# Performance work log

Measured on AMD Instinct MI355X. Metric: run time of the kernel, lower is better.

Reference implementation:

```python
import jax, jax.numpy as jnp
import numpy as np
from jax import lax

EPS = 1e-5

def _dsconv(x, dw, pw, g, b, m, v, relu):
    # x: [B,C,H,W]; dw: [C,1,3,3] depthwise; pw: [C,C,1,1] pointwise; eval-mode BN
    C = x.shape[1]
    y = lax.conv_general_dilated(x, dw, (1, 1), 'SAME', feature_group_count=C)
    y = lax.conv_general_dilated(y, pw, (1, 1), 'SAME')
    scale = (g * lax.rsqrt(v + EPS))[None, :, None, None]
    y = y * scale + (b - m * g * lax.rsqrt(v + EPS))[None, :, None, None]
    return jnp.maximum(y, 0.0) if relu else y

def _attention(x, wq, bq, wk, bk, wv, bv, gamma):
    b, c, h, w = x.shape
    n = h * w
    xf = x.reshape(b, c, n)                      # [B,C,N]
    q = jnp.einsum('oc,bcn->bon', wq, xf) + bq[None, :, None]   # [B,C/8,N]
    k = jnp.einsum('oc,bcn->bon', wk, xf) + bk[None, :, None]   # [B,C/8,N]
    v = jnp.einsum('oc,bcn->bon', wv, xf) + bv[None, :, None]   # [B,C,N]
    logits = jnp.einsum('bdm,bdn->bmn', q, k)    # q^T k, [B,N,N]
    attn = jax.nn.softmax(logits, axis=2)
    out = jnp.einsum('bcn,bmn->bcm', v, attn).reshape(b, c, h, w)
    return gamma[0] * out + x

def setup_inputs() -> dict:
    key = jax.random.key(0)
    ks = jax.random.split(key, 20)
    B, C, H, W = 64, 256, 32, 32
    C8 = C // 8
    rn = lambda k, s, sc: (jax.random.normal(k, s, dtype=jnp.float32) * sc)
    return {
        'x': rn(ks[0], (B, C, H, W), 1.0),
        'dw1': rn(ks[1], (C, 1, 3, 3), 0.2),
        'pw1': rn(ks[2], (C, C, 1, 1), 0.06),
        'bn1_g': jax.random.uniform(ks[3], (C,), jnp.float32, 0.5, 1.5),
        'bn1_b': rn(ks[4], (C,), 0.1),
        'bn1_m': rn(ks[5], (C,), 0.1),
        'bn1_v': jax.random.uniform(ks[6], (C,), jnp.float32, 0.5, 1.5),
        'dw2': rn(ks[7], (C, 1, 3, 3), 0.2),
        'pw2': rn(ks[8], (C, C, 1, 1), 0.06),
        'bn2_g': jax.random.uniform(ks[9], (C,), jnp.float32, 0.5, 1.5),
        'bn2_b': rn(ks[10], (C,), 0.1),
        'bn2_m': rn(ks[11], (C,), 0.1),
        'bn2_v': jax.random.uniform(ks[12], (C,), jnp.float32, 0.5, 1.5),
        'wq': rn(ks[13], (C8, C), 0.06),
        'bq': rn(ks[14], (C8,), 0.02),
        'wk': rn(ks[15], (C8, C), 0.06),
        'bk': rn(ks[16], (C8,), 0.02),
        'wv': rn(ks[17], (C, C), 0.06),
        'bv': rn(ks[18], (C,), 0.02),
        'gamma': rn(ks[19], (1,), 0.5),
    }

def reference(x, dw1, pw1, bn1_g, bn1_b, bn1_m, bn1_v,
              dw2, pw2, bn2_g, bn2_b, bn2_m, bn2_v,
              wq, bq, wk, bk, wv, bv, gamma):
    out = _dsconv(x, dw1, pw1, bn1_g, bn1_b, bn1_m, bn1_v, relu=True)
    out = _dsconv(out, dw2, pw2, bn2_g, bn2_b, bn2_m, bn2_v, relu=False)
    out = _attention(out + x, wq, bq, wk, bk, wv, bv, gamma)
    return jnp.maximum(out, 0.0)
```

## Files before the change

### kernel.cpp

```cpp
#include <hip/hip_runtime.h>
#include <cstdint>
#include <cstddef>

#define B_ 64
#define C_ 256
#define N_ 1024
#define LOG2E 1.4426950408889634f

typedef short v8s __attribute__((ext_vector_type(8)));
typedef float v4f __attribute__((ext_vector_type(4)));
typedef unsigned int u32;
typedef unsigned short u16;

__device__ __forceinline__ float bf2f(u16 u) {
  return __uint_as_float(((u32)u) << 16);
}
__device__ __forceinline__ u16 f2bf(float f) {
  u32 x = __float_as_uint(f);
  x += 0x7fffu + ((x >> 16) & 1u);
  return (u16)(x >> 16);
}
__device__ __forceinline__ u32 pack2(float a, float b) {
  return (u32)f2bf(a) | ((u32)f2bf(b) << 16);
}

typedef __attribute__((address_space(3))) unsigned int lds_as_t;
typedef __attribute__((address_space(1))) const unsigned int glb_as_t;
__device__ __forceinline__ void ld_lds16(const u16* g, u16* l) {
  __builtin_amdgcn_global_load_lds((glb_as_t*)g, (lds_as_t*)l, 16, 0, 0);
}

__global__ __launch_bounds__(256) void prep(
    const float* __restrict__ g1, const float* __restrict__ b1,
    const float* __restrict__ m1, const float* __restrict__ v1,
    const float* __restrict__ g2, const float* __restrict__ b2,
    const float* __restrict__ m2, const float* __restrict__ v2,
    const float* __restrict__ wq, const float* __restrict__ bq,
    const float* __restrict__ wk, const float* __restrict__ bk,
    const float* __restrict__ wv, const float* __restrict__ bv,
    const float* __restrict__ pw1, const float* __restrict__ pw2,
    const float* __restrict__ dw1, const float* __restrict__ dw2,
    float* __restrict__ scale1, float* __restrict__ shift1,
    float* __restrict__ scale2, float* __restrict__ shift2,
    float* __restrict__ dwT1, float* __restrict__ dwT2,
    u16* __restrict__ pw1b, u16* __restrict__ pw2b, u16* __restrict__ wcatb,
    float* __restrict__ bcat) {
  const int gt = blockIdx.x * 256 + threadIdx.x;
  if (gt < 256) {
    float s1 = g1[gt] * rsqrtf(v1[gt] + 1e-5f);
    scale1[gt] = s1;
    shift1[gt] = b1[gt] - m1[gt] * s1;
    float s2 = g2[gt] * rsqrtf(v2[gt] + 1e-5f);
    scale2[gt] = s2;
    shift2[gt] = b2[gt] - m2[gt] * s2;
  }
  if (gt < 320)
    bcat[gt] = (gt < 32) ? bq[gt] * LOG2E
                         : (gt < 64) ? bk[gt - 32] : bv[gt - 64];
  if (gt < 2304) {
    dwT1[(gt % 9) * 256 + gt / 9] = dw1[gt];
    dwT2[(gt % 9) * 256 + gt / 9] = dw2[gt];
  }
  for (int e = gt; e < 65536; e += 16384) {
    pw1b[e] = f2bf(pw1[e]);
    pw2b[e] = f2bf(pw2[e]);
  }
  for (int e = gt; e < 81920; e += 16384) {
    const int o = e >> 8;
    float w = (o < 32) ? wq[e] * LOG2E
                       : (o < 64) ? wk[e - 8192] : wv[e - 16384];
    wcatb[e] = f2bf(w);
  }
}

__global__ __launch_bounds__(256) void transpose_x(const float* __restrict__ x,
                                                   u16* __restrict__ xt) {
  __shared__ float t[64][65];
  const int b = blockIdx.z, c0 = blockIdx.y * 64, n0 = blockIdx.x * 64;
  const float* xp = x + ((size_t)b * C_ + c0) * N_ + n0;
  const int tn = threadIdx.x & 63, tc = threadIdx.x >> 6;
#pragma unroll
  for (int i = 0; i < 16; ++i)
    t[tc + 4 * i][tn] = xp[(size_t)(tc + 4 * i) * N_ + tn];
  __syncthreads();
  u16* op = xt + ((size_t)b * N_ + n0) * C_ + c0;
  const int oc = threadIdx.x & 63, on = threadIdx.x >> 6;
#pragma unroll
  for (int i = 0; i < 16; ++i)
    op[(size_t)(on + 4 * i) * C_ + oc] = f2bf(t[oc][on + 4 * i]);
}

__global__ __launch_bounds__(256) void dw_nhwc(const u16* __restrict__ src,
                                               const float* __restrict__ wT,
                                               u16* __restrict__ dst) {
  __shared__ float wl[9][256];
  const int b = blockIdx.y;
  for (int e = threadIdx.x; e < 2304; e += 256) wl[e >> 8][e & 255] = wT[e];
  __syncthreads();
  const int pl = threadIdx.x >> 5, c0 = (threadIdx.x & 31) * 8;
  const int p = blockIdx.x * 8 + pl;
  const int h = p >> 5, wx = p & 31;
  const u16* sp = src + (size_t)b * N_ * C_;
  float acc[8] = {0.f, 0.f, 0.f, 0.f, 0.f, 0.f, 0.f, 0.f};
#pragma unroll
  for (int dh = -1; dh <= 1; ++dh) {
    const int hh = h + dh;
    if (hh < 0 || hh > 31) continue;
#pragma unroll
    for (int dx = -1; dx <= 1; ++dx) {
      const int ww = wx + dx;
      if (ww < 0 || ww > 31) continue;
      const int k = (dh + 1) * 3 + (dx + 1);
      const uint4 v = *(const uint4*)(sp + (size_t)(hh * 32 + ww) * C_ + c0);
      const u32 vv[4] = {v.x, v.y, v.z, v.w};
#pragma unroll
      for (int j = 0; j < 4; ++j) {
        acc[2 * j] += bf2f((u16)(vv[j] & 0xffffu)) * wl[k][c0 + 2 * j];
        acc[2 * j + 1] += bf2f((u16)(vv[j] >> 16)) * wl[k][c0 + 2 * j + 1];
      }
    }
  }
  uint4 o4;
  o4.x = pack2(acc[0], acc[1]);
  o4.y = pack2(acc[2], acc[3]);
  o4.z = pack2(acc[4], acc[5]);
  o4.w = pack2(acc[6], acc[7]);
  *(uint4*)(dst + ((size_t)b * N_ + p) * C_ + c0) = o4;
}

template <int EPI>
__global__ __launch_bounds__(256) void gemm(
    const u16* __restrict__ X, const u16* __restrict__ W,
    const float* __restrict__ scale, const float* __restrict__ shift,
    const u16* __restrict__ resid, u16* __restrict__ Y, u16* __restrict__ Y2) {
  __shared__ u16 smem[17408];
  u16(*Xs)[64] = (u16(*)[64])smem;
  u16(*Ws)[64] = (u16(*)[64])(smem + 8192);
  u16(*Ys)[136] = (u16(*)[136])smem;

  const int tid = threadIdx.x;
  const int b = blockIdx.z;
  const int n0 = blockIdx.x * 128, o0 = blockIdx.y * 128;
  const int wid = tid >> 6, lane = tid & 63;
  const int wn = wid & 1, wo = wid >> 1;
  const int l15 = lane & 15, l4 = lane >> 4;
  const int lr = lane >> 3, lc = (lane & 7) * 8;

  v4f acc[4][4];
#pragma unroll
  for (int i = 0; i < 4; ++i)
#pragma unroll
    for (int j = 0; j < 4; ++j) acc[i][j] = v4f{0.f, 0.f, 0.f, 0.f};

  for (int k0 = 0; k0 < C_; k0 += 64) {
#pragma unroll
    for (int g = 0; g < 4; ++g) {
      const int base = wid * 32 + g * 8;
      ld_lds16(X + ((size_t)b * N_ + n0 + base + lr) * C_ + k0 + lc,
               &Xs[base][0]);
      int wr = o0 + base + lr;
      if (EPI == 2 && wr > 319) wr = 319;
      ld_lds16(W + (size_t)wr * C_ + k0 + lc, &Ws[base][0]);
    }
    __syncthreads();
#pragma unroll
    for (int ks = 0; ks < 2; ++ks) {
      v8s af[4], bf4[4];
#pragma unroll
      for (int f = 0; f < 4; ++f) {
        if constexpr (EPI != 2) {
          af[f] = *(const v8s*)&Ws[wo * 64 + f * 16 + l15][ks * 32 + l4 * 8];
          bf4[f] = *(const v8s*)&Xs[wn * 64 + f * 16 + l15][ks * 32 + l4 * 8];
        } else {
          af[f] = *(const v8s*)&Xs[wn * 64 + f * 16 + l15][ks * 32 + l4 * 8];
          bf4[f] = *(const v8s*)&Ws[wo * 64 + f * 16 + l15][ks * 32 + l4 * 8];
        }
      }
#pragma unroll
      for (int i = 0; i < 4; ++i)
#pragma unroll
        for (int j = 0; j < 4; ++j)
          acc[i][j] = __builtin_amdgcn_mfma_f32_16x16x32_bf16(
              af[i], bf4[j], acc[i][j], 0, 0, 0);
    }
    __syncthreads();
  }

  if constexpr (EPI != 2) {
#pragma unroll
    for (int i = 0; i < 4; ++i) {
      const int oL = wo * 64 + i * 16 + l4 * 4;
      const int o = o0 + oL;
      const float4 sc = *(const float4*)&scale[o];
      const float4 sh = *(const float4*)&shift[o];
#pragma unroll
      for (int j = 0; j < 4; ++j) {
        const int nL = wn * 64 + j * 16 + l15;
        float y0 = acc[i][j][0] * sc.x + sh.x;
        float y1 = acc[i][j][1] * sc.y + sh.y;
        float y2 = acc[i][j][2] * sc.z + sh.z;
        float y3 = acc[i][j][3] * sc.w + sh.w;
        if constexpr (EPI == 0) {
          y0 = fmaxf(y0, 0.f);
          y1 = fmaxf(y1, 0.f);
          y2 = fmaxf(y2, 0.f);
          y3 = fmaxf(y3, 0.f);
        } else {
          const uint2 rb =
              *(const uint2*)(resid + ((size_t)b * N_ + n0 + nL) * C_ + o);
          y0 += bf2f((u16)(rb.x & 0xffffu));
          y1 += bf2f((u16)(rb.x >> 16));
          y2 += bf2f((u16)(rb.y & 0xffffu));
          y3 += bf2f((u16)(rb.y >> 16));
        }
        uint2 st;
        st.x = pack2(y0, y1);
        st.y = pack2(y2, y3);
        *(uint2*)&Ys[nL][oL] = st;
      }
    }
    __syncthreads();
#pragma unroll
    for (int s = 0; s < 8; ++s) {
      const int nL = s * 16 + (tid >> 4);
      const int slot = tid & 15;
      const uint4 v = *(const uint4*)&Ys[nL][slot * 8];
      *(uint4*)&Y[((size_t)b * N_ + n0 + nL) * C_ + o0 + slot * 8] = v;
    }
  } else {
    float bj[4];
#pragma unroll
    for (int j = 0; j < 4; ++j) {
      int o = o0 + wo * 64 + j * 16 + l15;
      bj[j] = shift[o > 319 ? 319 : o];
    }
    if (o0 == 0 && wo == 0) {
#pragma unroll
      for (int i = 0; i < 4; ++i) {
        const int nB = n0 + wn * 64 + i * 16 + l4 * 4;
#pragma unroll
        for (int j = 0; j < 4; ++j) {
          const int o = j * 16 + l15;
#pragma unroll
          for (int r = 0; r < 4; ++r)
            Y[((size_t)b * N_ + nB + r) * 64 + o] = f2bf(acc[i][j][r] + bj[j]);
        }
      }
    } else {
#pragma unroll
      for (int i = 0; i < 4; ++i) {
        const int nL = wn * 64 + i * 16 + l4 * 4;
#pragma unroll
        for (int j = 0; j < 4; ++j) {
          const int oL = wo * 64 + j * 16 + l15;
          uint2 st;
          st.x = pack2(acc[i][j][0] + bj[j], acc[i][j][1] + bj[j]);
          st.y = pack2(acc[i][j][2] + bj[j], acc[i][j][3] + bj[j]);
          *(uint2*)&Ys[oL][nL] = st;
        }
      }
    }
    __syncthreads();
#pragma unroll
    for (int s = 0; s < 8; ++s) {
      const int oL = s * 16 + (tid >> 4);
      const int c = o0 + oL - 64;
      if (c >= 0 && c < 256) {
        const int slot = tid & 15;
        const uint4 v = *(const uint4*)&Ys[oL][slot * 8];
        *(uint4*)&Y2[((size_t)b * C_ + c) * N_ + n0 + slot * 8] = v;
      }
    }
  }
}

__global__ __launch_bounds__(256) void flash(const u16* __restrict__ qk,
                                             const u16* __restrict__ vchw,
                                             const u16* __restrict__ abf,
                                             const float* __restrict__ gamma_p,
                                             float* __restrict__ out) {
  const int b = blockIdx.x;
  const int m0 = blockIdx.y * 64;
  const int tid = threadIdx.x, wid = tid >> 6, lane = tid & 63;
  const int l15 = lane & 15, l4 = lane >> 4;
  const int mw = m0 + wid * 16;

  __shared__ u16 Vs[2][256][64];
  __shared__ u16 Plds[4][16][72];

  const u16* qkb = qk + (size_t)b * N_ * 64;
  const u16* vb = vchw + (size_t)b * C_ * N_;
  const v8s qf = *(const v8s*)&qkb[(size_t)(mw + l15) * 64 + l4 * 8];

  const int src_c = lane >> 3;
  const int src_j = (lane & 7) ^ (lane >> 3);

#pragma unroll
  for (int g = 0; g < 8; ++g) {
    const int base = wid * 64 + g * 8;
    ld_lds16(vb + (size_t)(base + src_c) * N_ + src_j * 8, &Vs[0][base][0]);
  }

  float Mloc = -3e38f;
  v8s kf[4];
#pragma unroll
  for (int f = 0; f < 4; ++f)
    kf[f] = *(const v8s*)&qkb[(size_t)(f * 16 + l15) * 64 + 32 + l4 * 8];
  for (int t = 0; t < 16; ++t) {
    v8s kn[4];
    if (t < 15) {
      const int n1 = (t + 1) * 64;
#pragma unroll
      for (int f = 0; f < 4; ++f)
        kn[f] =
            *(const v8s*)&qkb[(size_t)(n1 + f * 16 + l15) * 64 + 32 + l4 * 8];
    }
#pragma unroll
    for (int f = 0; f < 4; ++f) {
      const v4f lt = __builtin_amdgcn_mfma_f32_16x16x32_bf16(
          kf[f], qf, v4f{0.f, 0.f, 0.f, 0.f}, 0, 0, 0);
      Mloc = fmaxf(Mloc, fmaxf(fmaxf(lt[0], lt[1]), fmaxf(lt[2], lt[3])));
    }
    if (t < 15) {
#pragma unroll
      for (int f = 0; f < 4; ++f) kf[f] = kn[f];
    }
  }
  Mloc = fmaxf(Mloc, __shfl_xor(Mloc, 16));
  Mloc = fmaxf(Mloc, __shfl_xor(Mloc, 32));
  const float M = Mloc;

  v4f acc[16];
#pragma unroll
  for (int i = 0; i < 16; ++i) acc[i] = v4f{0.f, 0.f, 0.f, 0.f};
  float S0 = 0.f, S1 = 0.f, S2 = 0.f, S3 = 0.f;
#pragma unroll
  for (int f = 0; f < 4; ++f)
    kf[f] = *(const v8s*)&qkb[(size_t)(f * 16 + l15) * 64 + 32 + l4 * 8];
  __syncthreads();

  for (int t = 0; t < 16; ++t) {
    const int cur = t & 1;
    v4f lt[4];
#pragma unroll
    for (int f = 0; f < 4; ++f)
      lt[f] = __builtin_amdgcn_mfma_f32_16x16x32_bf16(
          kf[f], qf, v4f{0.f, 0.f, 0.f, 0.f}, 0, 0, 0);
    if (t < 15) {
      const int n1 = (t + 1) * 64;
#pragma unroll
      for (int g = 0; g < 8; ++g) {
        const int base = wid * 64 + g * 8;
        ld_lds16(vb + (size_t)(base + src_c) * N_ + n1 + src_j * 8,
                 &Vs[cur ^ 1][base][0]);
      }
#pragma unroll
      for (int f = 0; f < 4; ++f)
        kf[f] =
            *(const v8s*)&qkb[(size_t)(n1 + f * 16 + l15) * 64 + 32 + l4 * 8];
    }
#pragma unroll
    for (int f = 0; f < 4; ++f) {
      const float p0 = exp2f(lt[f][0] - M);
      const float p1 = exp2f(lt[f][1] - M);
      const float p2 = exp2f(lt[f][2] - M);
      const float p3 = exp2f(lt[f][3] - M);
      S0 += p0;
      S1 += p1;
      S2 += p2;
      S3 += p3;
      uint2 pw;
      pw.x = pack2(p0, p1);
      pw.y = pack2(p2, p3);
      *(uint2*)&Plds[wid][l15][f * 16 + l4 * 4] = pw;
    }
    __builtin_amdgcn_s_setprio(1);
#pragma unroll
    for (int ks = 0; ks < 2; ++ks) {
      const v8s pa = *(const v8s*)&Plds[wid][l15][ks * 32 + l4 * 8];
#pragma unroll
      for (int cf = 0; cf < 16; ++cf) {
        const int col = 8 * (((ks * 4) + l4) ^ (l15 & 7));
        const v8s vf = *(const v8s*)&Vs[cur][cf * 16 + l15][col];
        acc[cf] = __builtin_amdgcn_mfma_f32_16x16x32_bf16(pa, vf, acc[cf], 0,
                                                          0, 0);
      }
    }
    __builtin_amdgcn_s_setprio(0);
    __syncthreads();
  }

  float S = (S0 + S1) + (S2 + S3);
  S += __shfl_xor(S, 16);
  S += __shfl_xor(S, 32);
  const float inv = 1.f / S;
  const float g = gamma_p[0];
  float invr[4];
#pragma unroll
  for (int r = 0; r < 4; ++r) invr[r] = __shfl(inv, l4 * 4 + r);
  const int mb = mw + l4 * 4;
#pragma unroll
  for (int cf = 0; cf < 16; ++cf) {
    const int c = cf * 16 + l15;
    float4 y;
    float* yp = (float*)&y;
#pragma unroll
    for (int r = 0; r < 4; ++r) {
      const float av = bf2f(abf[((size_t)b * N_ + mb + r) * C_ + c]);
      yp[r] = fmaxf(g * acc[cf][r] * invr[r] + av, 0.f);
    }
    *(float4*)&out[((size_t)b * C_ + c) * N_ + mb] = y;
  }
}

extern "C" void kernel_launch(void* const* d_in, const int* in_sizes, int n_in,
                              void* d_out, int out_size, void* d_ws,
                              size_t ws_size, hipStream_t stream) {
  const float* x = (const float*)d_in[0];
  const float* dw1 = (const float*)d_in[1];
  const float* pw1 = (const float*)d_in[2];
  const float* bn1g = (const float*)d_in[3];
  const float* bn1b = (const float*)d_in[4];
  const float* bn1m = (const float*)d_in[5];
  const float* bn1v = (const float*)d_in[6];
  const float* dw2 = (const float*)d_in[7];
  const float* pw2 = (const float*)d_in[8];
  const float* bn2g = (const float*)d_in[9];
  const float* bn2b = (const float*)d_in[10];
  const float* bn2m = (const float*)d_in[11];
  const float* bn2v = (const float*)d_in[12];
  const float* wq = (const float*)d_in[13];
  const float* bq = (const float*)d_in[14];
  const float* wk = (const float*)d_in[15];
  const float* bk = (const float*)d_in[16];
  const float* wv = (const float*)d_in[17];
  const float* bv = (const float*)d_in[18];
  const float* gamma = (const float*)d_in[19];
  float* out = (float*)d_out;

  char* ws = (char*)d_ws;
  size_t off = 0;
  auto alloc = [&](size_t bytes) {
    void* p = ws + off;
    off += (bytes + 255) & ~(size_t)255;
    return p;
  };
  const size_t NE = (size_t)B_ * N_ * C_;

  u16* bufA = (u16*)alloc(NE * 2);
  u16* bufB = (u16*)alloc(NE * 2);
  u16* bufC = (u16*)alloc(NE * 2);
  u16* abf = (u16*)alloc(NE * 2);
  float* scale1 = (float*)alloc(256 * 4);
  float* shift1 = (float*)alloc(256 * 4);
  float* scale2 = (float*)alloc(256 * 4);
  float* shift2 = (float*)alloc(256 * 4);
  float* dwT1 = (float*)alloc(2304 * 4);
  float* dwT2 = (float*)alloc(2304 * 4);
  u16* pw1b = (u16*)alloc(65536 * 2);
  u16* pw2b = (u16*)alloc(65536 * 2);
  u16* wcatb = (u16*)alloc(81920 * 2);
  float* bcat = (float*)alloc(384 * 4);

  u16* xt = bufA;
  u16* t1 = bufB;
  u16* y1 = bufC;
  u16* t2 = bufB;
  u16* qkbuf = bufC;
  u16* vchw = bufA;

  prep<<<64, 256, 0, stream>>>(bn1g, bn1b, bn1m, bn1v, bn2g, bn2b, bn2m, bn2v,
                               wq, bq, wk, bk, wv, bv, pw1, pw2, dw1, dw2,
                               scale1, shift1, scale2, shift2, dwT1, dwT2,
                               pw1b, pw2b, wcatb, bcat);
  transpose_x<<<dim3(16, 4, B_), 256, 0, stream>>>(x, xt);
  dw_nhwc<<<dim3(128, B_), 256, 0, stream>>>(xt, dwT1, t1);
  gemm<0><<<dim3(8, 2, B_), 256, 0, stream>>>(t1, pw1b, scale1, shift1,
                                              nullptr, y1, nullptr);
  dw_nhwc<<<dim3(128, B_), 256, 0, stream>>>(y1, dwT2, t2);
  gemm<1><<<dim3(8, 2, B_), 256, 0, stream>>>(t2, pw2b, scale2, shift2, xt,
                                              abf, nullptr);
  gemm<2><<<dim3(8, 3, B_), 256, 0, stream>>>(abf, wcatb, nullptr, bcat,
                                              nullptr, qkbuf, vchw);
  flash<<<dim3(64, 16), 256, 0, stream>>>(qkbuf, vchw, abf, gamma, out);
}
```

Before: 258.2 us.

## Read V fragments directly from global memory in flash kernel and coalesce QK stores

The flash attention kernel no longer stages V tiles into double-buffered shared memory. Each wave now loads its V fragments straight from global memory (relying on L2/cache), which removes the LDS traffic and the per-iteration block barrier. The cost is that every wave reloads the same V data, so global and cache traffic rises and load latency is exposed inside the MFMA loop. Separately, the GEMM epilogue for the QK output now goes through shared memory so it can write 16-byte coalesced rows instead of scattered 2-byte stores.

```diff
diff --git a/kernel.cpp b/kernel.cpp
--- a/kernel.cpp
+++ b/kernel.cpp
@@ -137,6 +137,7 @@
   u16(*Xs)[64] = (u16(*)[64])smem;
   u16(*Ws)[64] = (u16(*)[64])(smem + 8192);
   u16(*Ys)[136] = (u16(*)[136])smem;
+  u16(*YsQ)[68] = (u16(*)[68])smem;
 
   const int tid = threadIdx.x;
   const int b = blockIdx.z;
@@ -237,13 +238,12 @@
     if (o0 == 0 && wo == 0) {
 #pragma unroll
       for (int i = 0; i < 4; ++i) {
-        const int nB = n0 + wn * 64 + i * 16 + l4 * 4;
+        const int nL = wn * 64 + i * 16 + l4 * 4;
 #pragma unroll
         for (int j = 0; j < 4; ++j) {
-          const int o = j * 16 + l15;
-#pragma unroll
-          for (int r = 0; r < 4; ++r)
-            Y[((size_t)b * N_ + nB + r) * 64 + o] = f2bf(acc[i][j][r] + bj[j]);
+          const int oL = j * 16 + l15;
+#pragma unroll
+          for (int r = 0; r < 4; ++r) YsQ[nL + r][oL] = f2bf(acc[i][j][r] + bj[j]);
         }
       }
     } else {
@@ -261,14 +261,31 @@
       }
     }
     __syncthreads();
-#pragma unroll
-    for (int s = 0; s < 8; ++s) {
-      const int oL = s * 16 + (tid >> 4);
-      const int c = o0 + oL - 64;
-      if (c >= 0 && c < 256) {
-        const int slot = tid & 15;
+    if (o0 == 0) {
+#pragma unroll
+      for (int s = 0; s < 4; ++s) {
+        const int e = s * 256 + tid;
+        const int row = e >> 3, seg = e & 7;
+        const uint4 v = *(const uint4*)&YsQ[row][seg * 8];
+        *(uint4*)&Y[((size_t)b * N_ + n0 + row) * 64 + seg * 8] = v;
+      }
+#pragma unroll
+      for (int s = 0; s < 4; ++s) {
+        const int e = s * 256 + tid;
+        const int oL = 64 + (e >> 4), slot = e & 15;
         const uint4 v = *(const uint4*)&Ys[oL][slot * 8];
-        *(uint4*)&Y2[((size_t)b * C_ + c) * N_ + n0 + slot * 8] = v;
+        *(uint4*)&Y2[((size_t)b * C_ + oL - 64) * N_ + n0 + slot * 8] = v;
+      }
+    } else {
+#pragma unroll
+      for (int s = 0; s < 8; ++s) {
+        const int oL = s * 16 + (tid >> 4);
+        const int c = o0 + oL - 64;
+        if (c < 256) {
+          const int slot = tid & 15;
+          const uint4 v = *(const uint4*)&Ys[oL][slot * 8];
+          *(uint4*)&Y2[((size_t)b * C_ + c) * N_ + n0 + slot * 8] = v;
+        }
       }
     }
   }
@@ -285,21 +302,11 @@
   const int l15 = lane & 15, l4 = lane >> 4;
   const int mw = m0 + wid * 16;
 
-  __shared__ u16 Vs[2][256][64];
   __shared__ u16 Plds[4][16][72];
 
   const u16* qkb = qk + (size_t)b * N_ * 64;
   const u16* vb = vchw + (size_t)b * C_ * N_;
   const v8s qf = *(const v8s*)&qkb[(size_t)(mw + l15) * 64 + l4 * 8];
-
-  const int src_c = lane >> 3;
-  const int src_j = (lane & 7) ^ (lane >> 3);
-
-#pragma unroll
-  for (int g = 0; g < 8; ++g) {
-    const int base = wid * 64 + g * 8;
-    ld_lds16(vb + (size_t)(base + src_c) * N_ + src_j * 8, &Vs[0][base][0]);
-  }
 
   float Mloc = -3e38f;
   v8s kf[4];
@@ -337,10 +344,8 @@
 #pragma unroll
   for (int f = 0; f < 4; ++f)
     kf[f] = *(const v8s*)&qkb[(size_t)(f * 16 + l15) * 64 + 32 + l4 * 8];
-  __syncthreads();
 
   for (int t = 0; t < 16; ++t) {
-    const int cur = t & 1;
     v4f lt[4];
 #pragma unroll
     for (int f = 0; f < 4; ++f)
@@ -348,12 +353,6 @@
           kf[f], qf, v4f{0.f, 0.f, 0.f, 0.f}, 0, 0, 0);
     if (t < 15) {
       const int n1 = (t + 1) * 64;
-#pragma unroll
-      for (int g = 0; g < 8; ++g) {
-        const int base = wid * 64 + g * 8;
-        ld_lds16(vb + (size_t)(base + src_c) * N_ + n1 + src_j * 8,
-                 &Vs[cur ^ 1][base][0]);
-      }
 #pragma unroll
       for (int f = 0; f < 4; ++f)
         kf[f] =
@@ -374,20 +373,20 @@
       pw.y = pack2(p2, p3);
       *(uint2*)&Plds[wid][l15][f * 16 + l4 * 4] = pw;
     }
+    const u16* vt = vb + t * 64 + l4 * 8;
     __builtin_amdgcn_s_setprio(1);
 #pragma unroll
     for (int ks = 0; ks < 2; ++ks) {
       const v8s pa = *(const v8s*)&Plds[wid][l15][ks * 32 + l4 * 8];
 #pragma unroll
       for (int cf = 0; cf < 16; ++cf) {
-        const int col = 8 * (((ks * 4) + l4) ^ (l15 & 7));
-        const v8s vf = *(const v8s*)&Vs[cur][cf * 16 + l15][col];
+        const v8s vf =
+            *(const v8s*)(vt + (size_t)(cf * 16 + l15) * N_ + ks * 32);
         acc[cf] = __builtin_amdgcn_mfma_f32_16x16x32_bf16(pa, vf, acc[cf], 0,
                                                           0, 0);
       }
     }
     __builtin_amdgcn_s_setprio(0);
-    __syncthreads();
   }
 
   float S = (S0 + S1) + (S2 + S3);
```

New measurement: 474.8 us. +83.9%, slower.
